# Kernel tuning notes

Hardware: AMD Instinct MI355X
Metric: run time of the kernel (lower is better)

## Reference

```python
import jax, jax.numpy as jnp
import numpy as np

B = 16384      # number of batched 6-node FC graphs
A = 6          # num_agents (nodes per graph)
D_OBS = 128    # raw observation dim
D_EMB = 250    # embedding / GAT feature dim
H = 3          # GAT heads (head outputs averaged to keep dim 250)
HID = 256
N_ACT = 5
NEG_SLOPE = 0.2


def setup_inputs() -> dict:
    key = jax.random.key(0)
    ks = jax.random.split(key, 16)
    def w(i, shape, scale=0.05):
        return jax.random.normal(ks[i], shape, dtype=jnp.float32) * scale
    return {
        "x": jax.random.normal(ks[0], (B * A, D_OBS), dtype=jnp.float32),
        "W_emb": w(1, (D_OBS, D_EMB)), "b_emb": jnp.zeros((D_EMB,), jnp.float32),
        "W_gat": w(2, (H, D_EMB, D_EMB)),
        "a_l": w(3, (H, D_EMB)), "a_r": w(4, (H, D_EMB)),
        "W1": w(5, (2 * D_EMB, HID)), "b1": jnp.zeros((HID,), jnp.float32),
        "W2": w(6, (HID, N_ACT)), "b2": jnp.zeros((N_ACT,), jnp.float32),
        "V1": w(7, (2 * D_EMB, HID)), "vb1": jnp.zeros((HID,), jnp.float32),
        "V2": w(8, (HID, 1)), "vb2": jnp.zeros((1,), jnp.float32),
    }


def reference(x, W_emb, b_emb, W_gat, a_l, a_r, W1, b1, W2, b2, V1, vb1, V2, vb2):
    # embedding layer
    h = jax.nn.relu(x @ W_emb + b_emb)                       # [N, 250]
    hb = h.reshape(B, A, D_EMB)                              # [B, 6, 250]
    # GAT on fully-connected 6-node graphs (incl. self edges), dense-masked form
    Wh = jnp.einsum("bad,hde->bhae", hb, W_gat)              # [B, H, 6, 250]
    el = jnp.einsum("bhae,he->bha", Wh, a_l)                 # dst term
    er = jnp.einsum("bhae,he->bha", Wh, a_r)                 # src term
    e = jax.nn.leaky_relu(el[:, :, :, None] + er[:, :, None, :], NEG_SLOPE)  # [B,H,6,6]
    attn = jax.nn.softmax(e, axis=-1)                        # edge softmax over neighbors
    gat = jnp.einsum("bhij,bhje->bhie", attn, Wh).mean(axis=1)  # mean over heads -> [B,6,250]
    feat = jnp.concatenate([hb, gat], axis=-1).reshape(B * A, 2 * D_EMB)  # [N, 500]
    # actor head (reg1)
    probs = jax.nn.softmax(jax.nn.relu(feat @ W1 + b1) @ W2 + b2, axis=-1)  # [N, 5]
    # critic head (reg2)
    value = jax.nn.relu(feat @ V1 + vb1) @ V2 + vb2           # [N, 1]
    return jnp.concatenate([probs, value], axis=-1)          # [N, 6]
```

## Files before the change

### kernel.cpp

```cpp
#include <hip/hip_runtime.h>

typedef unsigned short u16;
typedef unsigned int   u32;
typedef unsigned long long u64;
typedef __attribute__((ext_vector_type(4))) int   i32x4;
typedef __attribute__((ext_vector_type(4))) float f32x4;
typedef __attribute__((ext_vector_type(8))) short s16x8;

#define NROWS 98304L
#define LDF   512

__device__ __forceinline__ u16 f2bf(float x) {
  union { float f; u32 u; } v; v.f = x;
  return (u16)((v.u + 0x7FFFu + ((v.u >> 16) & 1u)) >> 16);
}
__device__ __forceinline__ float bf2f(u16 b) {
  union { float f; u32 u; } v; v.u = ((u32)b) << 16;
  return v.f;
}

__device__ __forceinline__ void gload_lds16(const u16* g, u16* l) {
  __builtin_amdgcn_global_load_lds(
      (const __attribute__((address_space(1))) unsigned int*)g,
      (__attribute__((address_space(3))) unsigned int*)l, 16, 0, 0);
}

__global__ __launch_bounds__(256)
void prep_weights(const float* __restrict__ W_emb, const float* __restrict__ b_emb,
                  const float* __restrict__ W_gat, const float* __restrict__ a_l,
                  const float* __restrict__ a_r, const float* __restrict__ W1,
                  const float* __restrict__ b1, const float* __restrict__ V1,
                  const float* __restrict__ vb1,
                  u16* __restrict__ Wemb_t, u16* __restrict__ Wgat_t,
                  u16* __restrict__ W1V1_t, float* __restrict__ bembp,
                  float* __restrict__ b1vb1)
{
  const int idx = blockIdx.x * 256 + threadIdx.x;
  const int stride = gridDim.x * 256;
  for (int t = idx; t < 256 * 128; t += stride) {
    int n = t >> 7, k = t & 127;
    Wemb_t[t] = f2bf(n < 250 ? W_emb[k * 250 + n] : 0.f);
  }
  for (int t = idx; t < 3 * 256 * 256; t += stride) {
    int h = t >> 16, rem = t & 65535, e = rem >> 8, d = rem & 255;
    float v = 0.f;
    if (e < 250 && d < 250) {
      v = W_gat[(h * 250 + d) * 250 + e];
    } else if ((e == 250 || e == 251) && d < 250) {
      const float* av = ((e == 250) ? a_l : a_r) + h * 250;
      const float* wrow = W_gat + ((long)h * 250 + d) * 250;
      float s = 0.f;
      for (int q = 0; q < 250; q++) s += wrow[q] * av[q];
      v = s;
    }
    Wgat_t[t] = f2bf(v);
  }
  for (int t = idx; t < 512 * 512; t += stride) {
    int n = t >> 9, k = t & 511;
    const float* src = (n < 256) ? W1 : V1;
    int col = n & 255;
    float v = 0.f;
    if (k < 250) v = src[k * 256 + col];
    else if (k >= 256 && k < 506) v = src[(k - 6) * 256 + col];
    W1V1_t[t] = f2bf(v);
  }
  for (int t = idx; t < 512; t += stride) b1vb1[t] = (t < 256) ? b1[t] : vb1[t - 256];
  for (int t = idx; t < 256; t += stride) bembp[t] = (t < 250) ? b_emb[t] : 0.f;
}

__global__ __launch_bounds__(256, 2)
void gemm1f(const float* __restrict__ X,
            const u16* __restrict__ B,
            u16* __restrict__ C,
            const float* __restrict__ bias)
{
  __shared__ __align__(16) u16 At[128 * 64];
  __shared__ __align__(16) u16 Bt[128 * 64];
  const int tid = threadIdx.x;
  const int w = tid >> 6, lane = tid & 63;
  const int fl = lane & 15, fh = lane >> 4;
  const int wr = (w >> 1) * 64, wc = (w & 1) * 64;
  const int srow = lane >> 3;
  const int slot = lane & 7;
  const int schunk = ((slot ^ srow) << 3);
  const int swz = (fl & 7) << 3;

  const int nidx = blockIdx.x;
  const int midx = blockIdx.y;

  const float* Ax = X + (long)midx * 128 * 128;
  const u16* Bb = B + nidx * 128 * 128;
  u16* Cb = C + (long)midx * 128 * LDF + nidx * 128;
  const float* biasb = bias + nidx * 128;

  f32x4 acc[4][4];
  #pragma unroll
  for (int m = 0; m < 4; m++)
    #pragma unroll
    for (int n = 0; n < 4; n++)
      acc[m][n] = f32x4{0.f, 0.f, 0.f, 0.f};

  for (int ks = 0; ks < 2; ks++) {
    __syncthreads();
    #pragma unroll
    for (int c = 0; c < 4; c++) {
      const int row = w * 32 + c * 8 + srow;
      gload_lds16(Bb + (long)row * 128 + ks * 64 + schunk, Bt + (w * 4 + c) * 512);
      const float* src = Ax + (long)row * 128 + ks * 64 + schunk;
      f32x4 lo = *(const f32x4*)src;
      f32x4 hi = *(const f32x4*)(src + 4);
      i32x4 o;
      o[0] = (int)((u32)f2bf(lo[0]) | ((u32)f2bf(lo[1]) << 16));
      o[1] = (int)((u32)f2bf(lo[2]) | ((u32)f2bf(lo[3]) << 16));
      o[2] = (int)((u32)f2bf(hi[0]) | ((u32)f2bf(hi[1]) << 16));
      o[3] = (int)((u32)f2bf(hi[2]) | ((u32)f2bf(hi[3]) << 16));
      *(i32x4*)(At + row * 64 + slot * 8) = o;
    }
    __syncthreads();
    #pragma unroll
    for (int kk = 0; kk < 2; kk++) {
      s16x8 af[4], bfr[4];
      #pragma unroll
      for (int m = 0; m < 4; m++)
        af[m] = *(const s16x8*)(At + (wr + m * 16 + fl) * 64 + ((kk * 32 + fh * 8) ^ swz));
      #pragma unroll
      for (int n = 0; n < 4; n++)
        bfr[n] = *(const s16x8*)(Bt + (wc + n * 16 + fl) * 64 + ((kk * 32 + fh * 8) ^ swz));
      #pragma unroll
      for (int m = 0; m < 4; m++)
        #pragma unroll
        for (int n = 0; n < 4; n++)
          acc[m][n] = __builtin_amdgcn_mfma_f32_16x16x32_bf16(af[m], bfr[n], acc[m][n], 0, 0, 0);
    }
  }
  #pragma unroll
  for (int m = 0; m < 4; m++) {
    const int r0 = wr + m * 16 + fh * 4;
    #pragma unroll
    for (int n = 0; n < 4; n++) {
      const int col = wc + n * 16 + fl;
      const float bvv = biasb[col];
      f32x4 v = acc[m][n];
      #pragma unroll
      for (int r = 0; r < 4; r++)
        Cb[(long)(r0 + r) * LDF + col] = f2bf(fmaxf(v[r] + bvv, 0.f));
    }
  }
}

template<int KSTEPS>
__global__ __launch_bounds__(256, 2)
void gemm_bf16(const u16* __restrict__ A, int lda,
               const u16* __restrict__ B, int ldb, long strideB,
               u16* __restrict__ C, int ldc, long strideC, int nb)
{
  __shared__ __align__(16) u16 At[128 * 64];
  __shared__ __align__(16) u16 Bt[128 * 64];
  const int tid = threadIdx.x;
  const int w = tid >> 6, lane = tid & 63;
  const int fl = lane & 15, fh = lane >> 4;
  const int wr = (w >> 1) * 64, wc = (w & 1) * 64;
  const int srow = lane >> 3;
  const int scol = (((lane & 7) ^ srow) << 3);
  const int swz = (fl & 7) << 3;

  const int nidx = blockIdx.x % nb;
  const int zidx = blockIdx.x / nb;
  const int midx = blockIdx.y;

  const u16* Ab = A + (long)midx * 128 * lda;
  const u16* Bb = B + (long)zidx * strideB + (long)nidx * 128 * ldb;
  u16* Cb = C + (long)zidx * strideC + (long)midx * 128 * ldc + nidx * 128;

  f32x4 acc[4][4];
  #pragma unroll
  for (int m = 0; m < 4; m++)
    #pragma unroll
    for (int n = 0; n < 4; n++)
      acc[m][n] = f32x4{0.f, 0.f, 0.f, 0.f};

  for (int ks = 0; ks < KSTEPS; ks++) {
    __syncthreads();
    #pragma unroll
    for (int c = 0; c < 4; c++) {
      const int row = w * 32 + c * 8 + srow;
      gload_lds16(Ab + (long)row * lda + ks * 64 + scol, At + (w * 4 + c) * 512);
      gload_lds16(Bb + (long)row * ldb + ks * 64 + scol, Bt + (w * 4 + c) * 512);
    }
    __syncthreads();
    #pragma unroll
    for (int kk = 0; kk < 2; kk++) {
      s16x8 af[4], bfr[4];
      #pragma unroll
      for (int m = 0; m < 4; m++)
        af[m] = *(const s16x8*)(At + (wr + m * 16 + fl) * 64 + ((kk * 32 + fh * 8) ^ swz));
      #pragma unroll
      for (int n = 0; n < 4; n++)
        bfr[n] = *(const s16x8*)(Bt + (wc + n * 16 + fl) * 64 + ((kk * 32 + fh * 8) ^ swz));
      #pragma unroll
      for (int m = 0; m < 4; m++)
        #pragma unroll
        for (int n = 0; n < 4; n++)
          acc[m][n] = __builtin_amdgcn_mfma_f32_16x16x32_bf16(af[m], bfr[n], acc[m][n], 0, 0, 0);
    }
  }
  #pragma unroll
  for (int m = 0; m < 4; m++) {
    const int r0 = wr + m * 16 + fh * 4;
    #pragma unroll
    for (int n = 0; n < 4; n++) {
      const int col = wc + n * 16 + fl;
      f32x4 v = acc[m][n];
      #pragma unroll
      for (int r = 0; r < 4; r++)
        Cb[(long)(r0 + r) * ldc + col] = f2bf(v[r]);
    }
  }
}

__global__ __launch_bounds__(256, 2)
void gemm3p(const u16* __restrict__ A,
            const u16* __restrict__ B,
            const float* __restrict__ b1vb1,
            const float* __restrict__ W2,
            const float* __restrict__ V2,
            float* __restrict__ partials)
{
  __shared__ __align__(16) u16 At[128 * 64];
  __shared__ __align__(16) u16 Bt[128 * 64];
  __shared__ float pstage[2][128][6];
  const int tid = threadIdx.x;
  const int w = tid >> 6, lane = tid & 63;
  const int fl = lane & 15, fh = lane >> 4;
  const int wr = (w >> 1) * 64, wc = (w & 1) * 64;
  const int wcid = w & 1;
  const int srow = lane >> 3;
  const int scol = (((lane & 7) ^ srow) << 3);
  const int swz = (fl & 7) << 3;

  const int nidx = blockIdx.x;
  const int midx = blockIdx.y;

  const u16* Ab = A + (long)midx * 128 * 512;
  const u16* Bb = B + (long)nidx * 128 * 512;

  f32x4 acc[4][4];
  #pragma unroll
  for (int m = 0; m < 4; m++)
    #pragma unroll
    for (int n = 0; n < 4; n++)
      acc[m][n] = f32x4{0.f, 0.f, 0.f, 0.f};

  for (int ks = 0; ks < 8; ks++) {
    __syncthreads();
    #pragma unroll
    for (int c = 0; c < 4; c++) {
      const int row = w * 32 + c * 8 + srow;
      gload_lds16(Ab + (long)row * 512 + ks * 64 + scol, At + (w * 4 + c) * 512);
      gload_lds16(Bb + (long)row * 512 + ks * 64 + scol, Bt + (w * 4 + c) * 512);
    }
    __syncthreads();
    #pragma unroll
    for (int kk = 0; kk < 2; kk++) {
      s16x8 af[4], bfr[4];
      #pragma unroll
      for (int m = 0; m < 4; m++)
        af[m] = *(const s16x8*)(At + (wr + m * 16 + fl) * 64 + ((kk * 32 + fh * 8) ^ swz));
      #pragma unroll
      for (int n = 0; n < 4; n++)
        bfr[n] = *(const s16x8*)(Bt + (wc + n * 16 + fl) * 64 + ((kk * 32 + fh * 8) ^ swz));
      #pragma unroll
      for (int m = 0; m < 4; m++)
        #pragma unroll
        for (int n = 0; n < 4; n++)
          acc[m][n] = __builtin_amdgcn_mfma_f32_16x16x32_bf16(af[m], bfr[n], acc[m][n], 0, 0, 0);
    }
  }

  float bv[4];
  #pragma unroll
  for (int n = 0; n < 4; n++) bv[n] = b1vb1[nidx * 128 + wc + n * 16 + fl];

  if (nidx < 2) {
    #pragma unroll
    for (int m = 0; m < 4; m++) {
      float ps[4][5];
      #pragma unroll
      for (int r = 0; r < 4; r++)
        #pragma unroll
        for (int j = 0; j < 5; j++) ps[r][j] = 0.f;
      #pragma unroll
      for (int n = 0; n < 4; n++) {
        const int gcol = nidx * 128 + wc + n * 16 + fl;
        float w2r[5];
        #pragma unroll
        for (int j = 0; j < 5; j++) w2r[j] = W2[gcol * 5 + j];
        #pragma unroll
        for (int r = 0; r < 4; r++) {
          float hid = fmaxf(acc[m][n][r] + bv[n], 0.f);
          #pragma unroll
          for (int j = 0; j < 5; j++) ps[r][j] += hid * w2r[j];
        }
      }
      #pragma unroll
      for (int off = 1; off < 16; off <<= 1)
        #pragma unroll
        for (int r = 0; r < 4; r++)
          #pragma unroll
          for (int j = 0; j < 5; j++) ps[r][j] += __shfl_xor(ps[r][j], off, 16);
      if (fl == 0) {
        const int row = wr + m * 16 + fh * 4;
        #pragma unroll
        for (int r = 0; r < 4; r++)
          #pragma unroll
          for (int j = 0; j < 5; j++) pstage[wcid][row + r][j] = ps[r][j];
      }
    }
  } else {
    #pragma unroll
    for (int m = 0; m < 4; m++) {
      float ps[4];
      #pragma unroll
      for (int r = 0; r < 4; r++) ps[r] = 0.f;
      #pragma unroll
      for (int n = 0; n < 4; n++) {
        const int gcol = nidx * 128 + wc + n * 16 + fl - 256;
        const float v2c = V2[gcol];
        #pragma unroll
        for (int r = 0; r < 4; r++)
          ps[r] += fmaxf(acc[m][n][r] + bv[n], 0.f) * v2c;
      }
      #pragma unroll
      for (int off = 1; off < 16; off <<= 1)
        #pragma unroll
        for (int r = 0; r < 4; r++) ps[r] += __shfl_xor(ps[r], off, 16);
      if (fl == 0) {
        const int row = wr + m * 16 + fh * 4;
        #pragma unroll
        for (int r = 0; r < 4; r++) pstage[wcid][row + r][5] = ps[r];
      }
    }
  }
  __syncthreads();

  if (tid < 128) {
    float* dst = partials + ((long)nidx * NROWS + (long)midx * 128 + tid) * 6;
    if (nidx < 2) {
      #pragma unroll
      for (int j = 0; j < 5; j++)
        dst[j] = pstage[0][tid][j] + pstage[1][tid][j];
    } else {
      dst[5] = pstage[0][tid][5] + pstage[1][tid][5];
    }
  }
}

__global__ __launch_bounds__(256)
void heads_final(const float* __restrict__ partials, const float* __restrict__ b2,
                 const float* __restrict__ vb2, float* __restrict__ out)
{
  const long row = (long)blockIdx.x * 256 + threadIdx.x;
  const long slab = NROWS * 6;
  const float* p = partials + row * 6;
  float lg[5];
  #pragma unroll
  for (int j = 0; j < 5; j++) lg[j] = p[j] + p[slab + j] + b2[j];
  const float val = p[2 * slab + 5] + p[3 * slab + 5] + vb2[0];
  float mx = -1e30f;
  #pragma unroll
  for (int j = 0; j < 5; j++) mx = fmaxf(mx, lg[j]);
  float s = 0.f, e[5];
  #pragma unroll
  for (int j = 0; j < 5; j++) { e[j] = __expf(lg[j] - mx); s += e[j]; }
  const float inv = 1.f / s;
  float* op = out + row * 6;
  #pragma unroll
  for (int j = 0; j < 5; j++) op[j] = e[j] * inv;
  op[5] = val;
}

__global__ __launch_bounds__(256)
void attn_gat(const u16* __restrict__ Wh, u16* __restrict__ feat)
{
  const int w = threadIdx.x >> 6, lane = threadIdx.x & 63;
  const long g = (long)blockIdx.x * 4 + w;
  const int c0 = lane * 4;

  u64 raw[3][6];
  #pragma unroll
  for (int h = 0; h < 3; h++)
    #pragma unroll
    for (int i = 0; i < 6; i++)
      raw[h][i] = *(const u64*)(Wh + (((long)h * NROWS + g * 6 + i) << 8) + c0);

  float gacc[6][4];
  #pragma unroll
  for (int i = 0; i < 6; i++)
    #pragma unroll
    for (int q = 0; q < 4; q++) gacc[i][q] = 0.f;

  #pragma unroll
  for (int h = 0; h < 3; h++) {
    float whf[6][4];
    #pragma unroll
    for (int i = 0; i < 6; i++) {
      u64 v = raw[h][i];
      whf[i][0] = bf2f((u16)v);
      whf[i][1] = bf2f((u16)(v >> 16));
      whf[i][2] = bf2f((u16)(v >> 32));
      whf[i][3] = bf2f((u16)(v >> 48));
    }
    float el[6], er[6];
    #pragma unroll
    for (int i = 0; i < 6; i++) {
      el[i] = __shfl(whf[i][2], 62, 64);
      er[i] = __shfl(whf[i][3], 62, 64);
    }
    #pragma unroll
    for (int i = 0; i < 6; i++) {
      float e[6]; float mx = -1e30f;
      #pragma unroll
      for (int j = 0; j < 6; j++) {
        float t = el[i] + er[j];
        t = (t > 0.f) ? t : 0.2f * t;
        e[j] = t; mx = fmaxf(mx, t);
      }
      float s = 0.f;
      #pragma unroll
      for (int j = 0; j < 6; j++) { e[j] = __expf(e[j] - mx); s += e[j]; }
      float inv = 1.f / s;
      #pragma unroll
      for (int j = 0; j < 6; j++) {
        float a = e[j] * inv;
        #pragma unroll
        for (int q = 0; q < 4; q++) gacc[i][q] += a * whf[j][q];
      }
    }
  }
  #pragma unroll
  for (int i = 0; i < 6; i++) {
    const float k = 1.f / 3.f;
    u64 o = (u64)f2bf(gacc[i][0] * k)
          | ((u64)f2bf(gacc[i][1] * k) << 16)
          | ((u64)f2bf(gacc[i][2] * k) << 32)
          | ((u64)f2bf(gacc[i][3] * k) << 48);
    *(u64*)(feat + (g * 6 + i) * LDF + 256 + c0) = o;
  }
}

extern "C" void kernel_launch(void* const* d_in, const int* in_sizes, int n_in,
                              void* d_out, int out_size, void* d_ws, size_t ws_size,
                              hipStream_t stream)
{
  const float* x     = (const float*)d_in[0];
  const float* W_emb = (const float*)d_in[1];
  const float* b_emb = (const float*)d_in[2];
  const float* W_gat = (const float*)d_in[3];
  const float* a_l   = (const float*)d_in[4];
  const float* a_r   = (const float*)d_in[5];
  const float* W1    = (const float*)d_in[6];
  const float* b1    = (const float*)d_in[7];
  const float* W2    = (const float*)d_in[8];
  const float* b2    = (const float*)d_in[9];
  const float* V1    = (const float*)d_in[10];
  const float* vb1   = (const float*)d_in[11];
  const float* V2    = (const float*)d_in[12];
  const float* vb2   = (const float*)d_in[13];

  char* ws = (char*)d_ws;
  u16* feat = (u16*)ws;
  char* r2  = ws + 100663296L;
  u16*   Whb      = (u16*)r2;
  float* partials = (float*)r2;
  char* wt  = r2 + 150994944L;
  u16*   Wemb_t = (u16*)wt;
  u16*   Wgat_t = (u16*)(wt + 65536);
  u16*   W1V1_t = (u16*)(wt + 458752);
  float* b1vb1  = (float*)(wt + 983040);
  float* bembp  = (float*)(wt + 985088);

  prep_weights<<<256, 256, 0, stream>>>(W_emb, b_emb, W_gat, a_l, a_r, W1, b1, V1, vb1,
                                        Wemb_t, Wgat_t, W1V1_t, bembp, b1vb1);
  gemm1f<<<dim3(2, 768), 256, 0, stream>>>(x, Wemb_t, feat, bembp);
  gemm_bf16<4><<<dim3(6, 768), 256, 0, stream>>>(feat, 512, Wgat_t, 256, 65536L,
                                                 Whb, 256, 25165824L, 2);
  attn_gat<<<4096, 256, 0, stream>>>(Whb, feat);
  gemm3p<<<dim3(4, 768), 256, 0, stream>>>(feat, W1V1_t, b1vb1, W2, V2, partials);
  heads_final<<<384, 256, 0, stream>>>(partials, b2, vb2, (float*)d_out);
}
```

Measured before the change: 364.4 us.

## Double-buffer LDS in head GEMM and reorder grids to iterate M fastest

The three GEMM launches now map blockIdx.x to the row (M) tile and blockIdx.y to the column/head tile. Consecutive blocks therefore share the same weight tile and walk through activations, which changes L2 reuse patterns. The head GEMM (gemm3p) also gets double-buffered LDS tiles, prefetching the next K-slice while MFMAs run on the current one, with one barrier per step instead of two. This doubles the LDS footprint of gemm3p, which may affect occupancy.

```diff
diff --git a/kernel.cpp b/kernel.cpp
--- a/kernel.cpp
+++ b/kernel.cpp
@@ -85,8 +85,8 @@
   const int schunk = ((slot ^ srow) << 3);
   const int swz = (fl & 7) << 3;
 
-  const int nidx = blockIdx.x;
-  const int midx = blockIdx.y;
+  const int midx = blockIdx.x;
+  const int nidx = blockIdx.y;
 
   const float* Ax = X + (long)midx * 128 * 128;
   const u16* Bb = B + nidx * 128 * 128;
@@ -152,7 +152,7 @@
 __global__ __launch_bounds__(256, 2)
 void gemm_bf16(const u16* __restrict__ A, int lda,
                const u16* __restrict__ B, int ldb, long strideB,
-               u16* __restrict__ C, int ldc, long strideC, int nb)
+               u16* __restrict__ C, int ldc, long strideC)
 {
   __shared__ __align__(16) u16 At[128 * 64];
   __shared__ __align__(16) u16 Bt[128 * 64];
@@ -164,9 +164,9 @@
   const int scol = (((lane & 7) ^ srow) << 3);
   const int swz = (fl & 7) << 3;
 
-  const int nidx = blockIdx.x % nb;
-  const int zidx = blockIdx.x / nb;
-  const int midx = blockIdx.y;
+  const int midx = blockIdx.x;
+  const int nidx = blockIdx.y & 1;
+  const int zidx = blockIdx.y >> 1;
 
   const u16* Ab = A + (long)midx * 128 * lda;
   const u16* Bb = B + (long)zidx * strideB + (long)nidx * 128 * ldb;
@@ -226,8 +226,8 @@
             const float* __restrict__ V2,
             float* __restrict__ partials)
 {
-  __shared__ __align__(16) u16 At[128 * 64];
-  __shared__ __align__(16) u16 Bt[128 * 64];
+  __shared__ __align__(16) u16 At[2][128 * 64];
+  __shared__ __align__(16) u16 Bt[2][128 * 64];
   __shared__ float pstage[2][128][6];
   const int tid = threadIdx.x;
   const int w = tid >> 6, lane = tid & 63;
@@ -238,8 +238,8 @@
   const int scol = (((lane & 7) ^ srow) << 3);
   const int swz = (fl & 7) << 3;
 
-  const int nidx = blockIdx.x;
-  const int midx = blockIdx.y;
+  const int midx = blockIdx.x;
+  const int nidx = blockIdx.y;
 
   const u16* Ab = A + (long)midx * 128 * 512;
   const u16* Bb = B + (long)nidx * 128 * 512;
@@ -251,30 +251,40 @@
     for (int n = 0; n < 4; n++)
       acc[m][n] = f32x4{0.f, 0.f, 0.f, 0.f};
 
+  #pragma unroll
+  for (int c = 0; c < 4; c++) {
+    const int row = w * 32 + c * 8 + srow;
+    gload_lds16(Ab + (long)row * 512 + scol, At[0] + (w * 4 + c) * 512);
+    gload_lds16(Bb + (long)row * 512 + scol, Bt[0] + (w * 4 + c) * 512);
+  }
+  __syncthreads();
+
   for (int ks = 0; ks < 8; ks++) {
-    __syncthreads();
-    #pragma unroll
-    for (int c = 0; c < 4; c++) {
-      const int row = w * 32 + c * 8 + srow;
-      gload_lds16(Ab + (long)row * 512 + ks * 64 + scol, At + (w * 4 + c) * 512);
-      gload_lds16(Bb + (long)row * 512 + ks * 64 + scol, Bt + (w * 4 + c) * 512);
-    }
-    __syncthreads();
+    const int cur = ks & 1;
+    if (ks < 7) {
+      #pragma unroll
+      for (int c = 0; c < 4; c++) {
+        const int row = w * 32 + c * 8 + srow;
+        gload_lds16(Ab + (long)row * 512 + (ks + 1) * 64 + scol, At[cur ^ 1] + (w * 4 + c) * 512);
+        gload_lds16(Bb + (long)row * 512 + (ks + 1) * 64 + scol, Bt[cur ^ 1] + (w * 4 + c) * 512);
+      }
+    }
     #pragma unroll
     for (int kk = 0; kk < 2; kk++) {
       s16x8 af[4], bfr[4];
       #pragma unroll
       for (int m = 0; m < 4; m++)
-        af[m] = *(const s16x8*)(At + (wr + m * 16 + fl) * 64 + ((kk * 32 + fh * 8) ^ swz));
+        af[m] = *(const s16x8*)(At[cur] + (wr + m * 16 + fl) * 64 + ((kk * 32 + fh * 8) ^ swz));
       #pragma unroll
       for (int n = 0; n < 4; n++)
-        bfr[n] = *(const s16x8*)(Bt + (wc + n * 16 + fl) * 64 + ((kk * 32 + fh * 8) ^ swz));
+        bfr[n] = *(const s16x8*)(Bt[cur] + (wc + n * 16 + fl) * 64 + ((kk * 32 + fh * 8) ^ swz));
       #pragma unroll
       for (int m = 0; m < 4; m++)
         #pragma unroll
         for (int n = 0; n < 4; n++)
           acc[m][n] = __builtin_amdgcn_mfma_f32_16x16x32_bf16(af[m], bfr[n], acc[m][n], 0, 0, 0);
     }
+    __syncthreads();
   }
 
   float bv[4];
@@ -481,10 +491,10 @@
 
   prep_weights<<<256, 256, 0, stream>>>(W_emb, b_emb, W_gat, a_l, a_r, W1, b1, V1, vb1,
                                         Wemb_t, Wgat_t, W1V1_t, bembp, b1vb1);
-  gemm1f<<<dim3(2, 768), 256, 0, stream>>>(x, Wemb_t, feat, bembp);
-  gemm_bf16<4><<<dim3(6, 768), 256, 0, stream>>>(feat, 512, Wgat_t, 256, 65536L,
-                                                 Whb, 256, 25165824L, 2);
+  gemm1f<<<dim3(768, 2), 256, 0, stream>>>(x, Wemb_t, feat, bembp);
+  gemm_bf16<4><<<dim3(768, 6), 256, 0, stream>>>(feat, 512, Wgat_t, 256, 65536L,
+                                                 Whb, 256, 25165824L);
   attn_gat<<<4096, 256, 0, stream>>>(Whb, feat);
-  gemm3p<<<dim3(4, 768), 256, 0, stream>>>(feat, W1V1_t, b1vb1, W2, V2, partials);
+  gemm3p<<<dim3(768, 4), 256, 0, stream>>>(feat, W1V1_t, b1vb1, W2, V2, partials);
   heads_final<<<384, 256, 0, stream>>>(partials, b2, vb2, (float*)d_out);
 }
```

Result: slower. 384.1 us (+5.4%).

## Raise gemm3p occupancy, swap grid order, restructure epilogue to cut registers

Applied to the files above, without the earlier changes.

The gemm3p launch bound goes from 2 to 4 blocks per CU. The epilogue now handles one actor output column at a time instead of holding a 4x5 partial array, which lowers register pressure. The grid is transposed so consecutive blocks walk the row tiles for one N tile, which changes the L2 reuse pattern (the A tile is no longer shared among adjacent blocks). Forcing 4 blocks per CU may cause spills given the 64-float accumulators, and the per-column loop adds more shuffle reductions.

```diff
diff --git a/kernel.cpp b/kernel.cpp
--- a/kernel.cpp
+++ b/kernel.cpp
@@ -218,7 +218,7 @@
   }
 }
 
-__global__ __launch_bounds__(256, 2)
+__global__ __launch_bounds__(256, 4)
 void gemm3p(const u16* __restrict__ A,
             const u16* __restrict__ B,
             const float* __restrict__ b1vb1,
@@ -238,8 +238,8 @@
   const int scol = (((lane & 7) ^ srow) << 3);
   const int swz = (fl & 7) << 3;
 
-  const int nidx = blockIdx.x;
-  const int midx = blockIdx.y;
+  const int midx = blockIdx.x;
+  const int nidx = blockIdx.y;
 
   const u16* Ab = A + (long)midx * 128 * 512;
   const u16* Bb = B + (long)nidx * 128 * 512;
@@ -281,63 +281,50 @@
   #pragma unroll
   for (int n = 0; n < 4; n++) bv[n] = b1vb1[nidx * 128 + wc + n * 16 + fl];
 
-  if (nidx < 2) {
-    #pragma unroll
-    for (int m = 0; m < 4; m++) {
-      float ps[4][5];
+  #pragma unroll
+  for (int m = 0; m < 4; m++) {
+    float hidv[4][4];
+    #pragma unroll
+    for (int n = 0; n < 4; n++)
       #pragma unroll
       for (int r = 0; r < 4; r++)
-        #pragma unroll
-        for (int j = 0; j < 5; j++) ps[r][j] = 0.f;
-      #pragma unroll
-      for (int n = 0; n < 4; n++) {
-        const int gcol = nidx * 128 + wc + n * 16 + fl;
-        float w2r[5];
-        #pragma unroll
-        for (int j = 0; j < 5; j++) w2r[j] = W2[gcol * 5 + j];
-        #pragma unroll
-        for (int r = 0; r < 4; r++) {
-          float hid = fmaxf(acc[m][n][r] + bv[n], 0.f);
+        hidv[n][r] = fmaxf(acc[m][n][r] + bv[n], 0.f);
+    const int row0 = wr + m * 16 + fh * 4;
+
+    if (nidx < 2) {
+      #pragma unroll
+      for (int j = 0; j < 5; j++) {
+        float ps[4] = {0.f, 0.f, 0.f, 0.f};
+        #pragma unroll
+        for (int n = 0; n < 4; n++) {
+          const float w2 = W2[(nidx * 128 + wc + n * 16 + fl) * 5 + j];
           #pragma unroll
-          for (int j = 0; j < 5; j++) ps[r][j] += hid * w2r[j];
+          for (int r = 0; r < 4; r++) ps[r] += hidv[n][r] * w2;
+        }
+        #pragma unroll
+        for (int off = 1; off < 16; off <<= 1)
+          #pragma unroll
+          for (int r = 0; r < 4; r++) ps[r] += __shfl_xor(ps[r], off, 16);
+        if (fl == 0) {
+          #pragma unroll
+          for (int r = 0; r < 4; r++) pstage[wcid][row0 + r][j] = ps[r];
         }
       }
-      #pragma unroll
-      for (int off = 1; off < 16; off <<= 1)
-        #pragma unroll
-        for (int r = 0; r < 4; r++)
-          #pragma unroll
-          for (int j = 0; j < 5; j++) ps[r][j] += __shfl_xor(ps[r][j], off, 16);
-      if (fl == 0) {
-        const int row = wr + m * 16 + fh * 4;
-        #pragma unroll
-        for (int r = 0; r < 4; r++)
-          #pragma unroll
-          for (int j = 0; j < 5; j++) pstage[wcid][row + r][j] = ps[r][j];
-      }
-    }
-  } else {
-    #pragma unroll
-    for (int m = 0; m < 4; m++) {
-      float ps[4];
-      #pragma unroll
-      for (int r = 0; r < 4; r++) ps[r] = 0.f;
+    } else {
+      float ps[4] = {0.f, 0.f, 0.f, 0.f};
       #pragma unroll
       for (int n = 0; n < 4; n++) {
-        const int gcol = nidx * 128 + wc + n * 16 + fl - 256;
-        const float v2c = V2[gcol];
-        #pragma unroll
-        for (int r = 0; r < 4; r++)
-          ps[r] += fmaxf(acc[m][n][r] + bv[n], 0.f) * v2c;
+        const float v2c = V2[nidx * 128 + wc + n * 16 + fl - 256];
+        #pragma unroll
+        for (int r = 0; r < 4; r++) ps[r] += hidv[n][r] * v2c;
       }
       #pragma unroll
       for (int off = 1; off < 16; off <<= 1)
         #pragma unroll
         for (int r = 0; r < 4; r++) ps[r] += __shfl_xor(ps[r], off, 16);
       if (fl == 0) {
-        const int row = wr + m * 16 + fh * 4;
-        #pragma unroll
-        for (int r = 0; r < 4; r++) pstage[wcid][row + r][5] = ps[r];
+        #pragma unroll
+        for (int r = 0; r < 4; r++) pstage[wcid][row0 + r][5] = ps[r];
       }
     }
   }
@@ -485,6 +472,6 @@
   gemm_bf16<4><<<dim3(6, 768), 256, 0, stream>>>(feat, 512, Wgat_t, 256, 65536L,
                                                  Whb, 256, 25165824L, 2);
   attn_gat<<<4096, 256, 0, stream>>>(Whb, feat);
-  gemm3p<<<dim3(4, 768), 256, 0, stream>>>(feat, W1V1_t, b1vb1, W2, V2, partials);
+  gemm3p<<<dim3(768, 4), 256, 0, stream>>>(feat, W1V1_t, b1vb1, W2, V2, partials);
   heads_final<<<384, 256, 0, stream>>>(partials, b2, vb2, (float*)d_out);
 }
```

After: 352.0 us. 1.04x faster.
